# Kernel tuning notes

Hardware: AMD Instinct MI355X
Metric: run time of the kernel (lower is better)

## Reference

```python
import jax, jax.numpy as jnp
import numpy as np

# Fixed multi-scale pyramid (H, W) per level -- static config, closed over.
SPATIAL_SHAPES = [(100, 100), (50, 50), (25, 25), (13, 13)]
D_MODEL, N_HEADS, N_LEVELS, N_POINTS = 256, 8, 4, 4
C_HEAD = D_MODEL // N_HEADS
B = 2
NUM_KEYS = sum(h * w for h, w in SPATIAL_SHAPES)  # 13294
NUM_QUERIES = NUM_KEYS


def setup_inputs() -> dict:
    key = jax.random.key(0)
    ks = jax.random.split(key, 12)
    d = D_MODEL
    return {
        "query": jax.random.normal(ks[0], (B, NUM_QUERIES, d), jnp.float32),
        "reference_points": jax.random.uniform(ks[1], (B, NUM_QUERIES, N_LEVELS, 2), jnp.float32),
        "input_flatten": jax.random.normal(ks[2], (B, NUM_KEYS, d), jnp.float32),
        "Wv": jax.random.normal(ks[3], (d, d), jnp.float32) * 0.02,
        "bv": jnp.zeros((d,), jnp.float32),
        "Ws": jax.random.normal(ks[4], (d, N_HEADS * N_LEVELS * N_POINTS * 2), jnp.float32) * 0.01,
        "bs": jax.random.normal(ks[5], (N_HEADS * N_LEVELS * N_POINTS * 2,), jnp.float32),
        "Wa": jax.random.normal(ks[6], (d, N_HEADS * N_LEVELS * N_POINTS), jnp.float32) * 0.02,
        "ba": jnp.zeros((N_HEADS * N_LEVELS * N_POINTS,), jnp.float32),
        "Wo": jax.random.normal(ks[7], (d, d), jnp.float32) * 0.02,
        "bo": jnp.zeros((d,), jnp.float32),
    }


def _bilinear_sample(v, grid, H, W):
    """torch.F.grid_sample(mode='bilinear', padding_mode='zeros', align_corners=False).
    v: (N, H, W, C); grid: (N, M, 2) with (x, y) in [-1, 1]. Returns (N, M, C)."""
    x = (grid[..., 0] + 1.0) * (W * 0.5) - 0.5
    y = (grid[..., 1] + 1.0) * (H * 0.5) - 0.5
    x0 = jnp.floor(x)
    y0 = jnp.floor(y)
    dx = x - x0
    dy = y - y0
    x0i = x0.astype(jnp.int32)
    y0i = y0.astype(jnp.int32)
    vflat = v.reshape(v.shape[0], H * W, v.shape[-1])

    def gather(xi, yi):
        valid = (xi >= 0) & (xi < W) & (yi >= 0) & (yi < H)
        idx = jnp.clip(yi, 0, H - 1) * W + jnp.clip(xi, 0, W - 1)  # (N, M)
        g = jnp.take_along_axis(vflat, idx[..., None], axis=1)
        return g * valid[..., None]

    v00 = gather(x0i, y0i)
    v10 = gather(x0i + 1, y0i)
    v01 = gather(x0i, y0i + 1)
    v11 = gather(x0i + 1, y0i + 1)
    return (v00 * ((1 - dx) * (1 - dy))[..., None]
            + v10 * (dx * (1 - dy))[..., None]
            + v01 * ((1 - dx) * dy)[..., None]
            + v11 * (dx * dy)[..., None])


def _ms_deform_attn(value, sampling_locations, attention_weights):
    # value: (B, NK, H, Ch); loc: (B, NQ, H, L, P, 2); w: (B, NQ, H, L, P)
    grids = 2.0 * sampling_locations - 1.0
    splits = np.cumsum([h * w for h, w in SPATIAL_SHAPES])[:-1]
    value_list = jnp.split(value, splits, axis=1)
    acc = 0.0
    for lvl, (H, W) in enumerate(SPATIAL_SHAPES):
        # (B, H*W, heads, Ch) -> (B*heads, H, W, Ch)
        v_l = value_list[lvl].reshape(B, H, W, N_HEADS, C_HEAD)
        v_l = v_l.transpose(0, 3, 1, 2, 4).reshape(B * N_HEADS, H, W, C_HEAD)
        # (B, NQ, heads, P, 2) -> (B*heads, NQ*P, 2)
        g_l = grids[:, :, :, lvl].transpose(0, 2, 1, 3, 4).reshape(B * N_HEADS, -1, 2)
        samp = _bilinear_sample(v_l, g_l, H, W)  # (B*heads, NQ*P, Ch)
        samp = samp.reshape(B, N_HEADS, -1, N_POINTS, C_HEAD)
        w_l = attention_weights[:, :, :, lvl].transpose(0, 2, 1, 3)  # (B, heads, NQ, P)
        acc = acc + jnp.einsum("bhqpc,bhqp->bhqc", samp, w_l)
    return acc.transpose(0, 2, 1, 3).reshape(B, -1, D_MODEL)  # (B, NQ, d_model)


def reference(query, reference_points, input_flatten, Wv, bv, Ws, bs, Wa, ba, Wo, bo):
    value = (input_flatten @ Wv + bv).reshape(B, NUM_KEYS, N_HEADS, C_HEAD)
    offsets = (query @ Ws + bs).reshape(B, NUM_QUERIES, N_HEADS, N_LEVELS, N_POINTS, 2)
    attw = jax.nn.softmax(
        (query @ Wa + ba).reshape(B, NUM_QUERIES, N_HEADS, N_LEVELS * N_POINTS), axis=-1
    ).reshape(B, NUM_QUERIES, N_HEADS, N_LEVELS, N_POINTS)
    # NOTE: module divides by [H, W] (not [W, H]) -- replicated faithfully.
    normalizer = jnp.asarray(SPATIAL_SHAPES, jnp.float32)  # (L, 2) = (H, W)
    normalizer = jnp.clip(normalizer, 1.0)
    loc = reference_points[:, :, None, :, None, :] + offsets / normalizer[None, None, None, :, None, :]
    out = _ms_deform_attn(value, loc, attw)
    return out @ Wo + bo
```

## Files before the change

### kernel.cpp

```cpp
#include <hip/hip_runtime.h>
#include <hip/hip_bf16.h>
#include <hip/hip_fp16.h>
#include <math.h>

#define B_  2
#define NQ  13294
#define NK  13294
#define M_  (B_ * NK)
#define MT  32
#define GX  ((M_ + MT - 1) / MT)

typedef __bf16 bf16x8 __attribute__((ext_vector_type(8)));
typedef float f32x4 __attribute__((ext_vector_type(4)));

static __device__ __forceinline__ f32x4 mfma16(bf16x8 a, bf16x8 b, f32x4 c) {
  return __builtin_amdgcn_mfma_f32_16x16x32_bf16(a, b, c, 0, 0, 0);
}

static __device__ __forceinline__ void pack_one(
    const float* __restrict__ W1, const float* __restrict__ W2,
    int N1, int Ntot, __hip_bfloat16* __restrict__ out, int g) {
  int lane = g & 63;
  int n_sub = (g >> 6) & 3;
  int kt = (g >> 8) & 7;
  int bn = g >> 11;
  int n = bn * 64 + n_sub * 16 + (lane & 15);
  int k0 = kt * 32 + (lane >> 4) * 8;
  const float* src; int nn, Ns;
  if (n < N1) { src = W1; nn = n; Ns = N1; }
  else        { src = W2; nn = n - N1; Ns = Ntot - N1; }
  bf16x8 v;
#pragma unroll
  for (int j = 0; j < 8; ++j) v[j] = (__bf16)src[(size_t)(k0 + j) * Ns + nn];
  *(bf16x8*)(out + (size_t)g * 8) = v;
}

__global__ __launch_bounds__(256) void pack_all(
    const float* __restrict__ Wv, const float* __restrict__ Ws,
    const float* __restrict__ Wa, const float* __restrict__ Wo,
    __hip_bfloat16* __restrict__ wv_p, __hip_bfloat16* __restrict__ wsa_p,
    __hip_bfloat16* __restrict__ wo_p) {
  const int b = blockIdx.x, t = threadIdx.x;
  if (b < 32)       pack_one(Wv, Wv, 256, 256, wv_p,  b * 256 + t);
  else if (b < 80)  pack_one(Ws, Wa, 256, 384, wsa_p, (b - 32) * 256 + t);
  else              pack_one(Wo, Wo, 256, 256, wo_p,  (b - 80) * 256 + t);
}

static __device__ __forceinline__ int bin_of(const float* refp, int b, int q) {
  const size_t base = (((size_t)b * NQ + q) * 4) * 2;
  float rx = refp[base + 0], ry = refp[base + 1];
  int bx = (int)(rx * 32.f); bx = bx < 0 ? 0 : (bx > 31 ? 31 : bx);
  int by = (int)(ry * 32.f); by = by < 0 ? 0 : (by > 31 ? 31 : by);
  return b * 1024 + by * 32 + bx;
}

__global__ __launch_bounds__(256) void hist_k(
    const float* __restrict__ refp, unsigned int* __restrict__ hist) {
  int i = blockIdx.x * 256 + threadIdx.x;
  if (i >= 2 * NQ) return;
  int b = i >= NQ; int q = i - b * NQ;
  atomicAdd(&hist[bin_of(refp, b, q)], 1u);
}

__global__ __launch_bounds__(256) void scan_k(
    const unsigned int* __restrict__ hist, unsigned int* __restrict__ cursor) {
  __shared__ unsigned int lds[256];
  const int t = threadIdx.x;
  unsigned int v[8], s = 0;
#pragma unroll
  for (int j = 0; j < 8; ++j) { v[j] = hist[t * 8 + j]; s += v[j]; }
  lds[t] = s; __syncthreads();
  for (int off = 1; off < 256; off <<= 1) {
    unsigned int x = (t >= off) ? lds[t - off] : 0u;
    __syncthreads();
    lds[t] += x;
    __syncthreads();
  }
  unsigned int base = lds[t] - s;
#pragma unroll
  for (int j = 0; j < 8; ++j) { cursor[t * 8 + j] = base; base += v[j]; }
}

__global__ __launch_bounds__(256) void scatter_k(
    const float* __restrict__ refp, unsigned int* __restrict__ cursor,
    unsigned int* __restrict__ perm) {
  int i = blockIdx.x * 256 + threadIdx.x;
  if (i >= 2 * NQ) return;
  int b = i >= NQ; int q = i - b * NQ;
  unsigned int pos = atomicAdd(&cursor[bin_of(refp, b, q)], 1u);
  perm[pos] = (unsigned int)q;
}

#define CSTR 68

__global__ __launch_bounds__(128) void gemm_mt(
    const float* __restrict__ inpf, const float* __restrict__ query,
    const bf16x8* __restrict__ wv_p, const bf16x8* __restrict__ wsa_p,
    const float* __restrict__ bv, const float* __restrict__ bs,
    const float* __restrict__ ba,
    __hip_bfloat16* __restrict__ value, __half* __restrict__ params) {
  __shared__ bf16x8 As[8 * 2 * 64];
  __shared__ float  Cs[2 * MT * CSTR];

  const int t = threadIdx.x;
  const int bm = blockIdx.x * MT;
  const int lane = t & 63, wid = t >> 6;
  const int mode = blockIdx.y;

  {
    const int r = t >> 2;
    const int row = bm + r;
    const int sm = r >> 4;
    const int lb = r & 15;
    const bool ok = row < M_;
    const float* Af = (mode == 0) ? inpf : query;
    const float* ap = Af + (size_t)row * 256 + (t & 3) * 64;
#pragma unroll
    for (int gi = 0; gi < 8; ++gi) {
      float4 u = make_float4(0.f,0.f,0.f,0.f), v = make_float4(0.f,0.f,0.f,0.f);
      if (ok) { u = *(const float4*)(ap + gi * 8); v = *(const float4*)(ap + gi * 8 + 4); }
      bf16x8 w;
      w[0]=(__bf16)u.x; w[1]=(__bf16)u.y; w[2]=(__bf16)u.z; w[3]=(__bf16)u.w;
      w[4]=(__bf16)v.x; w[5]=(__bf16)v.y; w[6]=(__bf16)v.z; w[7]=(__bf16)v.w;
      int k8 = (t & 3) * 8 + gi;
      As[((k8 >> 2) * 2 + sm) * 64 + lb + ((k8 & 3) << 4)] = w;
    }
  }
  __syncthreads();

  const bf16x8* Bp = (mode == 0) ? wv_p : wsa_p;
  const int NB = (mode == 1) ? 6 : 4;
  float* Cw = &Cs[wid * MT * CSTR];

  for (int nb = wid; nb < NB; nb += 2) {
    const int colbase = nb * 64;
    const bf16x8* bpn = Bp + (size_t)nb * 2048;

    f32x4 acc[2][4] = {};
#pragma unroll
    for (int kt = 0; kt < 8; ++kt) {
      bf16x8 a0 = As[(kt * 2 + 0) * 64 + lane];
      bf16x8 a1 = As[(kt * 2 + 1) * 64 + lane];
#pragma unroll
      for (int n = 0; n < 4; ++n) {
        bf16x8 b = bpn[(kt * 4 + n) * 64 + lane];
        acc[0][n] = mfma16(a0, b, acc[0][n]);
        acc[1][n] = mfma16(a1, b, acc[1][n]);
      }
    }

#pragma unroll
    for (int m = 0; m < 2; ++m)
#pragma unroll
      for (int n = 0; n < 4; ++n)
#pragma unroll
        for (int rg = 0; rg < 4; ++rg)
          Cw[(m * 16 + (lane >> 4) * 4 + rg) * CSTR + n * 16 + (lane & 15)] = acc[m][n][rg];

    if (mode == 0) {
#pragma unroll
      for (int p = 0; p < 4; ++p) {
        const int r = (lane >> 3) + p * 8;
        const int c = (lane & 7) * 8;
        const int row = bm + r;
        float4 u = *(float4*)&Cw[r * CSTR + c];
        float4 v = *(float4*)&Cw[r * CSTR + c + 4];
        const float* bias = bv + colbase + c;
        bf16x8 o;
        o[0]=(__bf16)(u.x+bias[0]); o[1]=(__bf16)(u.y+bias[1]);
        o[2]=(__bf16)(u.z+bias[2]); o[3]=(__bf16)(u.w+bias[3]);
        o[4]=(__bf16)(v.x+bias[4]); o[5]=(__bf16)(v.y+bias[5]);
        o[6]=(__bf16)(v.z+bias[6]); o[7]=(__bf16)(v.w+bias[7]);
        if (row < M_)
          *(bf16x8*)(value + (size_t)row * 256 + colbase + c) = o;
      }
    } else {
#pragma unroll
      for (int p = 0; p < 8; ++p) {
        const int r = (lane >> 4) + p * 4;
        const int c = (lane & 15) * 4;
        const int row = bm + r;
        const int col = colbase + c;
        float4 u = *(float4*)&Cw[r * CSTR + c];
        const float* bias = (col < 256) ? (bs + col) : (ba + col - 256);
        u.x += bias[0]; u.y += bias[1]; u.z += bias[2]; u.w += bias[3];
        if (row < M_) {
          __half2 h0 = __floats2half2_rn(u.x, u.y);
          __half2 h1 = __floats2half2_rn(u.z, u.w);
          uint2 st;
          st.x = *(unsigned int*)&h0;
          st.y = *(unsigned int*)&h1;
          *(uint2*)(params + (size_t)row * 384 + col) = st;
        }
      }
    }
  }
}

#define CS 65
#define REGH (64 * CS)

__global__ __launch_bounds__(256) void sampler(
    const float* __restrict__ refp, const __half* __restrict__ params,
    const __hip_bfloat16* __restrict__ value, const bf16x8* __restrict__ wo_p,
    const float* __restrict__ bo, const unsigned int* __restrict__ perm,
    float* __restrict__ outp) {
  __shared__ unsigned int combo[REGH];
  __shared__ bf16x8 accs[32][16];
  __shared__ unsigned int qmap[16];

  const int c  = blockIdx.x & 7;
  const int kk = blockIdx.x >> 3;
  const int bb = c >> 2;
  const int qb = (c & 3) * 208 + kk;
  if (qb > 830) return;
  const int q0 = qb * 16;

  const int t = threadIdx.x;
  if (t < 16)
    qmap[t] = (q0 + t < NQ) ? perm[(size_t)bb * NQ + q0 + t] : 0xFFFFFFFFu;
  __syncthreads();

  const int cqi = t >> 5;
  const int chh = (t >> 2) & 7;
  const int cl  = t & 3;

  const int lane = t & 63;
  const int wid  = t >> 6;
  const int q2   = lane >> 5;
  const int gh   = (lane >> 2) & 7;
  const int gs   = lane & 3;
  const char* vb = (const char*)value;
  const unsigned int voff0 = (unsigned int)bb * (NK * 512u) + (unsigned)(gh * 64 + gs * 16);

  const float DIMF[4]  = {100.f, 50.f, 25.f, 13.f};
  const int   LSTART[4] = {0, 10000, 12500, 13125};
  const float dimf  = DIMF[cl];
  const int   Wd    = (int)dimf;
  const int   lbase = LSTART[cl];

  for (int qc = 0; qc < 16; qc += 8) {
    {
      const unsigned int qreal = qmap[qc + cqi];
      const bool valid = qreal != 0xFFFFFFFFu;
      const size_t row = (size_t)bb * NQ + (valid ? qreal : 0);
      const __half* pr = params + row * 384;

      union { uint4 u[2]; __half h[16]; } LG;
      LG.u[0] = *(const uint4*)(pr + 256 + chh * 16);
      LG.u[1] = *(const uint4*)(pr + 256 + chh * 16 + 8);
      float lgf[16];
#pragma unroll
      for (int j = 0; j < 16; ++j) lgf[j] = __half2float(LG.h[j]);
      float m = lgf[0];
#pragma unroll
      for (int j = 1; j < 16; ++j) m = fmaxf(m, lgf[j]);
      float s = 0.f;
#pragma unroll
      for (int j = 0; j < 16; ++j) s += __expf(lgf[j] - m);
      const float inv = valid ? 1.f / s : 0.f;

      const float rx = refp[(row * 4 + cl) * 2 + 0];
      const float ry = refp[(row * 4 + cl) * 2 + 1];
      union { uint4 u; __half h[8]; } OF;
      OF.u = *(const uint4*)(pr + chh * 32 + cl * 8);
      unsigned int* cb = &combo[(cqi * 8 + chh) * CS + cl * 16];

#pragma unroll
      for (int p = 0; p < 4; ++p) {
        const float wa = __expf(lgf[cl * 4 + p] - m) * inv;
        const float x = rx * dimf + __half2float(OF.h[p * 2 + 0]) - 0.5f;
        const float y = ry * dimf + __half2float(OF.h[p * 2 + 1]) - 0.5f;
        const float xf = floorf(x), yf = floorf(y);
        const float dx = x - xf, dy = y - yf;
        const int x0 = (int)xf, y0 = (int)yf;
        float w00 = (1.f - dx) * (1.f - dy) * wa;
        float w10 = dx * (1.f - dy) * wa;
        float w01 = (1.f - dx) * dy * wa;
        float w11 = dx * dy * wa;
        int i0, i1, i2, i3, xi, yi;
        xi = x0;     yi = y0;
        if (xi >= 0 && xi < Wd && yi >= 0 && yi < Wd) i0 = lbase + yi * Wd + xi; else { i0 = 0; w00 = 0.f; }
        xi = x0 + 1; yi = y0;
        if (xi >= 0 && xi < Wd && yi >= 0 && yi < Wd) i1 = lbase + yi * Wd + xi; else { i1 = 0; w10 = 0.f; }
        xi = x0;     yi = y0 + 1;
        if (xi >= 0 && xi < Wd && yi >= 0 && yi < Wd) i2 = lbase + yi * Wd + xi; else { i2 = 0; w01 = 0.f; }
        xi = x0 + 1; yi = y0 + 1;
        if (xi >= 0 && xi < Wd && yi >= 0 && yi < Wd) i3 = lbase + yi * Wd + xi; else { i3 = 0; w11 = 0.f; }
        cb[p * 4 + 0] = ((__float_as_uint(w00) + 0x8000u) & 0xffff0000u) | (unsigned)i0;
        cb[p * 4 + 1] = ((__float_as_uint(w10) + 0x8000u) & 0xffff0000u) | (unsigned)i1;
        cb[p * 4 + 2] = ((__float_as_uint(w01) + 0x8000u) & 0xffff0000u) | (unsigned)i2;
        cb[p * 4 + 3] = ((__float_as_uint(w11) + 0x8000u) & 0xffff0000u) | (unsigned)i3;
      }
    }
    __syncthreads();

    {
      const int qw = wid * 2 + q2;
      const int rr = qw * 8 + gh;
      const unsigned int* cb = &combo[rr * CS];
      float a0=0.f,a1=0.f,a2=0.f,a3=0.f,a4=0.f,a5=0.f,a6=0.f,a7=0.f;
#pragma unroll 8
      for (int e = 0; e < 64; ++e) {
        const unsigned int u = cb[e];
        const float w = __uint_as_float(u & 0xffff0000u);
        const unsigned int voff = voff0 + ((u & 0xffffu) << 9);
        const uint4 v = *(const uint4*)(vb + (size_t)voff);
        a0 += w * __uint_as_float(v.x << 16);
        a1 += w * __uint_as_float(v.x & 0xffff0000u);
        a2 += w * __uint_as_float(v.y << 16);
        a3 += w * __uint_as_float(v.y & 0xffff0000u);
        a4 += w * __uint_as_float(v.z << 16);
        a5 += w * __uint_as_float(v.z & 0xffff0000u);
        a6 += w * __uint_as_float(v.w << 16);
        a7 += w * __uint_as_float(v.w & 0xffff0000u);
      }
      bf16x8 o;
      o[0]=(__bf16)a0; o[1]=(__bf16)a1; o[2]=(__bf16)a2; o[3]=(__bf16)a3;
      o[4]=(__bf16)a4; o[5]=(__bf16)a5; o[6]=(__bf16)a6; o[7]=(__bf16)a7;
      accs[gh * 4 + gs][qc + qw] = o;
    }
    __syncthreads();
  }

  {
    const bf16x8* bpn = wo_p + (size_t)wid * 2048;
    f32x4 oacc[4] = {};
#pragma unroll
    for (int kt = 0; kt < 8; ++kt) {
      bf16x8 a = accs[kt * 4 + (lane >> 4)][lane & 15];
#pragma unroll
      for (int n = 0; n < 4; ++n)
        oacc[n] = mfma16(a, bpn[(kt * 4 + n) * 64 + lane], oacc[n]);
    }
#pragma unroll
    for (int n = 0; n < 4; ++n) {
      const int col = wid * 64 + n * 16 + (lane & 15);
      const float bias = bo[col];
#pragma unroll
      for (int rg = 0; rg < 4; ++rg) {
        const int ql = (lane >> 4) * 4 + rg;
        const unsigned int qreal = qmap[ql];
        if (qreal != 0xFFFFFFFFu)
          outp[((size_t)bb * NQ + qreal) * 256 + col] = oacc[n][rg] + bias;
      }
    }
  }
}

extern "C" void kernel_launch(void* const* d_in, const int* in_sizes, int n_in,
                              void* d_out, int out_size, void* d_ws, size_t ws_size,
                              hipStream_t stream) {
  const float* query = (const float*)d_in[0];
  const float* refp  = (const float*)d_in[1];
  const float* inpf  = (const float*)d_in[2];
  const float* Wv    = (const float*)d_in[3];
  const float* bv    = (const float*)d_in[4];
  const float* Ws    = (const float*)d_in[5];
  const float* bs    = (const float*)d_in[6];
  const float* Wa    = (const float*)d_in[7];
  const float* ba    = (const float*)d_in[8];
  const float* Wo    = (const float*)d_in[9];
  const float* bo    = (const float*)d_in[10];
  float* out = (float*)d_out;

  char* w = (char*)d_ws;
  __hip_bfloat16* value  = (__hip_bfloat16*)w;            w += (size_t)M_ * 256 * 2;
  __half*         params = (__half*)w;                    w += (size_t)M_ * 384 * 2;
  __hip_bfloat16* wv_p   = (__hip_bfloat16*)w;            w += 256 * 256 * 2;
  __hip_bfloat16* wsa_p  = (__hip_bfloat16*)w;            w += 256 * 384 * 2;
  __hip_bfloat16* wo_p   = (__hip_bfloat16*)w;            w += 256 * 256 * 2;
  unsigned int*   hist   = (unsigned int*)w;              w += 2048 * 4;
  unsigned int*   cursor = (unsigned int*)w;              w += 2048 * 4;
  unsigned int*   perm   = (unsigned int*)w;

  hipMemsetAsync(hist, 0, 2048 * 4, stream);

  const int sg = (2 * NQ + 255) / 256;
  hist_k<<<sg, 256, 0, stream>>>(refp, hist);
  scan_k<<<1, 256, 0, stream>>>(hist, cursor);
  scatter_k<<<sg, 256, 0, stream>>>(refp, cursor, perm);

  pack_all<<<112, 256, 0, stream>>>(Wv, Ws, Wa, Wo, wv_p, wsa_p, wo_p);

  gemm_mt<<<dim3(GX, 2), 128, 0, stream>>>(
      inpf, query, (const bf16x8*)wv_p, (const bf16x8*)wsa_p,
      bv, bs, ba, value, params);

  sampler<<<1664, 256, 0, stream>>>(refp, params, value,
                                    (const bf16x8*)wo_p, bo, perm, out);
}
```

Before: 120.8 us.

## Pair horizontal bilinear taps and process all 16 queries per sampler block

The sampler now runs 512 threads and handles all 16 queries of a tile in a single pass instead of two 8-query iterations. Each bilinear row pair of horizontal neighbours is encoded as one index plus two packed bf16 weights, so the gather loop does 32 iterations with two adjacent 16-byte value loads each. This halves LDS metadata traffic and the per-tap index math. The sampled results reuse the combo shared buffer for the Wo MFMA stage, which is now split across 8 waves. The value buffer gets one padding row so the x+1 tap at the last key cannot read out of bounds. In exchange, the larger block raises register and LDS pressure per block.

```diff
diff --git a/kernel.cpp b/kernel.cpp
--- a/kernel.cpp
+++ b/kernel.cpp
@@ -197,23 +197,20 @@
   }
 }
 
-#define CS 65
-#define REGH (64 * CS)
-
-__global__ __launch_bounds__(256) void sampler(
+#define CS 66
+
+__global__ __launch_bounds__(512, 8) void sampler(
     const float* __restrict__ refp, const __half* __restrict__ params,
     const __hip_bfloat16* __restrict__ value, const bf16x8* __restrict__ wo_p,
     const float* __restrict__ bo, const unsigned int* __restrict__ perm,
     float* __restrict__ outp) {
-  __shared__ unsigned int combo[REGH];
-  __shared__ bf16x8 accs[32][16];
+  __shared__ unsigned int combo[128 * CS];
   __shared__ unsigned int qmap[16];
 
   const int c  = blockIdx.x & 7;
   const int kk = blockIdx.x >> 3;
   const int bb = c >> 2;
   const int qb = (c & 3) * 208 + kk;
-  if (qb > 830) return;
   const int q0 = qb * 16;
 
   const int t = threadIdx.x;
@@ -221,126 +218,142 @@
     qmap[t] = (q0 + t < NQ) ? perm[(size_t)bb * NQ + q0 + t] : 0xFFFFFFFFu;
   __syncthreads();
 
-  const int cqi = t >> 5;
-  const int chh = (t >> 2) & 7;
-  const int cl  = t & 3;
+  {
+    const int cqi = t >> 5;
+    const int chh = (t >> 2) & 7;
+    const int cl  = t & 3;
+    const float DIMF[4]  = {100.f, 50.f, 25.f, 13.f};
+    const int   LSTART[4] = {0, 10000, 12500, 13125};
+    const float dimf  = DIMF[cl];
+    const int   Wd    = (int)dimf;
+    const int   lbase = LSTART[cl];
+
+    const unsigned int qreal = qmap[cqi];
+    const bool valid = qreal != 0xFFFFFFFFu;
+    const size_t row = (size_t)bb * NQ + (valid ? qreal : 0);
+    const __half* pr = params + row * 384;
+
+    union { uint4 u[2]; __half h[16]; } LG;
+    LG.u[0] = *(const uint4*)(pr + 256 + chh * 16);
+    LG.u[1] = *(const uint4*)(pr + 256 + chh * 16 + 8);
+    float lgf[16];
+#pragma unroll
+    for (int j = 0; j < 16; ++j) lgf[j] = __half2float(LG.h[j]);
+    float m = lgf[0];
+#pragma unroll
+    for (int j = 1; j < 16; ++j) m = fmaxf(m, lgf[j]);
+    float s = 0.f;
+#pragma unroll
+    for (int j = 0; j < 16; ++j) s += __expf(lgf[j] - m);
+    const float inv = valid ? 1.f / s : 0.f;
+
+    const float rx = refp[(row * 4 + cl) * 2 + 0];
+    const float ry = refp[(row * 4 + cl) * 2 + 1];
+    union { uint4 u; __half h[8]; } OF;
+    OF.u = *(const uint4*)(pr + chh * 32 + cl * 8);
+    unsigned int* cb = &combo[(cqi * 8 + chh) * CS + cl * 16];
+
+#pragma unroll
+    for (int p = 0; p < 4; ++p) {
+      const float wa = __expf(lgf[cl * 4 + p] - m) * inv;
+      const float x = rx * dimf + __half2float(OF.h[p * 2 + 0]) - 0.5f;
+      const float y = ry * dimf + __half2float(OF.h[p * 2 + 1]) - 0.5f;
+      const float xf = floorf(x), yf = floorf(y);
+      const float dx = x - xf, dy = y - yf;
+      const int x0 = (int)xf, y0 = (int)yf;
+
+      float wxl = 1.f - dx, wxh = dx;
+      int xa;
+      if (x0 >= 0 && x0 <= Wd - 2)      { xa = x0; }
+      else if (x0 == -1)                { xa = 0;      wxl = dx;       wxh = 0.f; }
+      else if (x0 == Wd - 1)            { xa = Wd - 2; wxl = 0.f;      wxh = 1.f - dx; }
+      else                              { xa = 0;      wxl = 0.f;      wxh = 0.f; }
+
+#pragma unroll
+      for (int r = 0; r < 2; ++r) {
+        const int yr = y0 + r;
+        const float wy = r ? dy : (1.f - dy);
+        const bool vy = (yr >= 0) && (yr < Wd);
+        const float wl = vy ? wa * wy * wxl : 0.f;
+        const float wh = vy ? wa * wy * wxh : 0.f;
+        const int idx = lbase + (vy ? yr : 0) * Wd + xa;
+        const unsigned int w2 = ((__float_as_uint(wl) + 0x8000u) & 0xffff0000u)
+                              | ((__float_as_uint(wh) + 0x8000u) >> 16);
+        cb[(p * 2 + r) * 2 + 0] = w2;
+        cb[(p * 2 + r) * 2 + 1] = (unsigned)idx;
+      }
+    }
+  }
+  __syncthreads();
 
   const int lane = t & 63;
   const int wid  = t >> 6;
-  const int q2   = lane >> 5;
-  const int gh   = (lane >> 2) & 7;
-  const int gs   = lane & 3;
-  const char* vb = (const char*)value;
-  const unsigned int voff0 = (unsigned int)bb * (NK * 512u) + (unsigned)(gh * 64 + gs * 16);
-
-  const float DIMF[4]  = {100.f, 50.f, 25.f, 13.f};
-  const int   LSTART[4] = {0, 10000, 12500, 13125};
-  const float dimf  = DIMF[cl];
-  const int   Wd    = (int)dimf;
-  const int   lbase = LSTART[cl];
-
-  for (int qc = 0; qc < 16; qc += 8) {
-    {
-      const unsigned int qreal = qmap[qc + cqi];
-      const bool valid = qreal != 0xFFFFFFFFu;
-      const size_t row = (size_t)bb * NQ + (valid ? qreal : 0);
-      const __half* pr = params + row * 384;
-
-      union { uint4 u[2]; __half h[16]; } LG;
-      LG.u[0] = *(const uint4*)(pr + 256 + chh * 16);
-      LG.u[1] = *(const uint4*)(pr + 256 + chh * 16 + 8);
-      float lgf[16];
-#pragma unroll
-      for (int j = 0; j < 16; ++j) lgf[j] = __half2float(LG.h[j]);
-      float m = lgf[0];
-#pragma unroll
-      for (int j = 1; j < 16; ++j) m = fmaxf(m, lgf[j]);
-      float s = 0.f;
-#pragma unroll
-      for (int j = 0; j < 16; ++j) s += __expf(lgf[j] - m);
-      const float inv = valid ? 1.f / s : 0.f;
-
-      const float rx = refp[(row * 4 + cl) * 2 + 0];
-      const float ry = refp[(row * 4 + cl) * 2 + 1];
-      union { uint4 u; __half h[8]; } OF;
-      OF.u = *(const uint4*)(pr + chh * 32 + cl * 8);
-      unsigned int* cb = &combo[(cqi * 8 + chh) * CS + cl * 16];
-
-#pragma unroll
-      for (int p = 0; p < 4; ++p) {
-        const float wa = __expf(lgf[cl * 4 + p] - m) * inv;
-        const float x = rx * dimf + __half2float(OF.h[p * 2 + 0]) - 0.5f;
-        const float y = ry * dimf + __half2float(OF.h[p * 2 + 1]) - 0.5f;
-        const float xf = floorf(x), yf = floorf(y);
-        const float dx = x - xf, dy = y - yf;
-        const int x0 = (int)xf, y0 = (int)yf;
-        float w00 = (1.f - dx) * (1.f - dy) * wa;
-        float w10 = dx * (1.f - dy) * wa;
-        float w01 = (1.f - dx) * dy * wa;
-        float w11 = dx * dy * wa;
-        int i0, i1, i2, i3, xi, yi;
-        xi = x0;     yi = y0;
-        if (xi >= 0 && xi < Wd && yi >= 0 && yi < Wd) i0 = lbase + yi * Wd + xi; else { i0 = 0; w00 = 0.f; }
-        xi = x0 + 1; yi = y0;
-        if (xi >= 0 && xi < Wd && yi >= 0 && yi < Wd) i1 = lbase + yi * Wd + xi; else { i1 = 0; w10 = 0.f; }
-        xi = x0;     yi = y0 + 1;
-        if (xi >= 0 && xi < Wd && yi >= 0 && yi < Wd) i2 = lbase + yi * Wd + xi; else { i2 = 0; w01 = 0.f; }
-        xi = x0 + 1; yi = y0 + 1;
-        if (xi >= 0 && xi < Wd && yi >= 0 && yi < Wd) i3 = lbase + yi * Wd + xi; else { i3 = 0; w11 = 0.f; }
-        cb[p * 4 + 0] = ((__float_as_uint(w00) + 0x8000u) & 0xffff0000u) | (unsigned)i0;
-        cb[p * 4 + 1] = ((__float_as_uint(w10) + 0x8000u) & 0xffff0000u) | (unsigned)i1;
-        cb[p * 4 + 2] = ((__float_as_uint(w01) + 0x8000u) & 0xffff0000u) | (unsigned)i2;
-        cb[p * 4 + 3] = ((__float_as_uint(w11) + 0x8000u) & 0xffff0000u) | (unsigned)i3;
-      }
-    }
-    __syncthreads();
-
-    {
-      const int qw = wid * 2 + q2;
-      const int rr = qw * 8 + gh;
-      const unsigned int* cb = &combo[rr * CS];
-      float a0=0.f,a1=0.f,a2=0.f,a3=0.f,a4=0.f,a5=0.f,a6=0.f,a7=0.f;
-#pragma unroll 8
-      for (int e = 0; e < 64; ++e) {
-        const unsigned int u = cb[e];
-        const float w = __uint_as_float(u & 0xffff0000u);
-        const unsigned int voff = voff0 + ((u & 0xffffu) << 9);
-        const uint4 v = *(const uint4*)(vb + (size_t)voff);
-        a0 += w * __uint_as_float(v.x << 16);
-        a1 += w * __uint_as_float(v.x & 0xffff0000u);
-        a2 += w * __uint_as_float(v.y << 16);
-        a3 += w * __uint_as_float(v.y & 0xffff0000u);
-        a4 += w * __uint_as_float(v.z << 16);
-        a5 += w * __uint_as_float(v.z & 0xffff0000u);
-        a6 += w * __uint_as_float(v.w << 16);
-        a7 += w * __uint_as_float(v.w & 0xffff0000u);
-      }
-      bf16x8 o;
-      o[0]=(__bf16)a0; o[1]=(__bf16)a1; o[2]=(__bf16)a2; o[3]=(__bf16)a3;
-      o[4]=(__bf16)a4; o[5]=(__bf16)a5; o[6]=(__bf16)a6; o[7]=(__bf16)a7;
-      accs[gh * 4 + gs][qc + qw] = o;
-    }
-    __syncthreads();
-  }
 
   {
-    const bf16x8* bpn = wo_p + (size_t)wid * 2048;
-    f32x4 oacc[4] = {};
+    const int q2 = lane >> 5;
+    const int gh = (lane >> 2) & 7;
+    const int gs = lane & 3;
+    const int qw = wid * 2 + q2;
+    const int rr = qw * 8 + gh;
+    const char* vb = (const char*)value;
+    const unsigned int voff0 = (unsigned int)bb * (NK * 512u) + (unsigned)(gh * 64 + gs * 16);
+    const uint2* cb = (const uint2*)&combo[rr * CS];
+
+    float a0=0.f,a1=0.f,a2=0.f,a3=0.f,a4=0.f,a5=0.f,a6=0.f,a7=0.f;
+#pragma unroll 4
+    for (int e = 0; e < 32; ++e) {
+      const uint2 u = cb[e];
+      const float wl = __uint_as_float(u.x & 0xffff0000u);
+      const float wh = __uint_as_float(u.x << 16);
+      const char* pv = vb + (size_t)(voff0 + (u.y << 9));
+      const uint4 v0 = *(const uint4*)(pv);
+      const uint4 v1 = *(const uint4*)(pv + 512);
+      a0 += wl * __uint_as_float(v0.x << 16);
+      a1 += wl * __uint_as_float(v0.x & 0xffff0000u);
+      a2 += wl * __uint_as_float(v0.y << 16);
+      a3 += wl * __uint_as_float(v0.y & 0xffff0000u);
+      a4 += wl * __uint_as_float(v0.z << 16);
+      a5 += wl * __uint_as_float(v0.z & 0xffff0000u);
+      a6 += wl * __uint_as_float(v0.w << 16);
+      a7 += wl * __uint_as_float(v0.w & 0xffff0000u);
+      a0 += wh * __uint_as_float(v1.x << 16);
+      a1 += wh * __uint_as_float(v1.x & 0xffff0000u);
+      a2 += wh * __uint_as_float(v1.y << 16);
+      a3 += wh * __uint_as_float(v1.y & 0xffff0000u);
+      a4 += wh * __uint_as_float(v1.z << 16);
+      a5 += wh * __uint_as_float(v1.z & 0xffff0000u);
+      a6 += wh * __uint_as_float(v1.w << 16);
+      a7 += wh * __uint_as_float(v1.w & 0xffff0000u);
+    }
+    bf16x8 o;
+    o[0]=(__bf16)a0; o[1]=(__bf16)a1; o[2]=(__bf16)a2; o[3]=(__bf16)a3;
+    o[4]=(__bf16)a4; o[5]=(__bf16)a5; o[6]=(__bf16)a6; o[7]=(__bf16)a7;
+    *(bf16x8*)(&combo[rr * CS + (rr & 1) * 2 + gs * 4]) = o;
+  }
+  __syncthreads();
+
+  {
+    const int ql = lane & 15;
+    const int hi = lane >> 4;
+    const unsigned int* abase = combo + ql * (8 * CS) + hi * 4;
+    const int cbk = wid >> 1, sp = wid & 1;
+    const bf16x8* bpn = wo_p + (size_t)cbk * 2048;
+    f32x4 oacc[2] = {};
 #pragma unroll
     for (int kt = 0; kt < 8; ++kt) {
-      bf16x8 a = accs[kt * 4 + (lane >> 4)][lane & 15];
-#pragma unroll
-      for (int n = 0; n < 4; ++n)
-        oacc[n] = mfma16(a, bpn[(kt * 4 + n) * 64 + lane], oacc[n]);
-    }
-#pragma unroll
-    for (int n = 0; n < 4; ++n) {
-      const int col = wid * 64 + n * 16 + (lane & 15);
+      bf16x8 a = *(const bf16x8*)(abase + kt * CS + (kt & 1) * 2);
+#pragma unroll
+      for (int n = 0; n < 2; ++n)
+        oacc[n] = mfma16(a, bpn[(kt * 4 + sp * 2 + n) * 64 + lane], oacc[n]);
+    }
+#pragma unroll
+    for (int n = 0; n < 2; ++n) {
+      const int col = cbk * 64 + sp * 32 + n * 16 + ql;
       const float bias = bo[col];
 #pragma unroll
       for (int rg = 0; rg < 4; ++rg) {
-        const int ql = (lane >> 4) * 4 + rg;
-        const unsigned int qreal = qmap[ql];
+        const int qi = hi * 4 + rg;
+        const unsigned int qreal = qmap[qi];
         if (qreal != 0xFFFFFFFFu)
           outp[((size_t)bb * NQ + qreal) * 256 + col] = oacc[n][rg] + bias;
       }
@@ -365,7 +378,7 @@
   float* out = (float*)d_out;
 
   char* w = (char*)d_ws;
-  __hip_bfloat16* value  = (__hip_bfloat16*)w;            w += (size_t)M_ * 256 * 2;
+  __hip_bfloat16* value  = (__hip_bfloat16*)w;            w += (size_t)(M_ + 1) * 256 * 2;
   __half*         params = (__half*)w;                    w += (size_t)M_ * 384 * 2;
   __hip_bfloat16* wv_p   = (__hip_bfloat16*)w;            w += 256 * 256 * 2;
   __hip_bfloat16* wsa_p  = (__hip_bfloat16*)w;            w += 256 * 384 * 2;
@@ -387,6 +400,6 @@
       inpf, query, (const bf16x8*)wv_p, (const bf16x8*)wsa_p,
       bv, bs, ba, value, params);
 
-  sampler<<<1664, 256, 0, stream>>>(refp, params, value,
+  sampler<<<1664, 512, 0, stream>>>(refp, params, value,
                                     (const bf16x8*)wo_p, bo, perm, out);
 }
```

After: 129.3 us. 7.0% more time.
